# Kernel optimization log

Hardware: AMD Instinct MI355X
Metric: run time of the kernel (lower is better)

The kernel has to match this reference:

```python
import jax, jax.numpy as jnp
import numpy as np

DIM = 512; H = 8; TEMP_LEN = 16; TARGET_LEN = 22
NT = TEMP_LEN ** 2          # 256 temp tokens
NS = TARGET_LEN ** 2        # 484 target tokens
N = NT + NS                 # 740
HD = DIM // H
SCALE = HD ** -0.5
EPS = 1e-5
B = 16


def _bias_index(L):
    coords = np.stack(np.meshgrid(np.arange(L), np.arange(L), indexing='ij')).reshape(2, -1)
    rel = (coords[:, :, None] - coords[:, None, :]).transpose(1, 2, 0)  # [L^2, L^2, 2]
    rel[..., 0] += L - 1
    rel[..., 1] += L - 1
    rel[..., 0] *= 2 * L - 1
    return jnp.asarray(rel.sum(-1))  # [L^2, L^2] indices into (2L-1)^2 table

TEMP_IDX = _bias_index(TEMP_LEN)
TARGET_IDX = _bias_index(TARGET_LEN)


def setup_inputs() -> dict:
    key = jax.random.key(0)
    ctr = iter(range(100))
    def nrm(shape, s=1.0):
        return jax.random.normal(jax.random.fold_in(key, next(ctr)), shape, jnp.float32) * s
    def uni(shape):
        return jax.random.uniform(jax.random.fold_in(key, next(ctr)), shape, jnp.float32, 0.5, 1.5)
    d = {'x': nrm((B, N, DIM))}
    for nm in ('q', 'k', 'v'):
        d[f'conv_{nm}_w'] = nrm((DIM, 1, 3, 3), 0.2)   # depthwise 3x3, groups=DIM
        d[f'bn_{nm}_g'] = 1.0 + nrm((DIM,), 0.1)
        d[f'bn_{nm}_b'] = nrm((DIM,), 0.1)
        d[f'bn_{nm}_m'] = nrm((DIM,), 0.1)
        d[f'bn_{nm}_v'] = uni((DIM,))
    for nm in ('q', 'k', 'v', 'p'):
        d[f'w{nm}'] = nrm((DIM, DIM), DIM ** -0.5)
        d[f'b{nm}'] = nrm((DIM,), 0.01)
    d['rpb_target'] = nrm(((2 * TARGET_LEN - 1) ** 2, H), 0.0002)
    d['rpb_temp'] = nrm(((2 * TEMP_LEN - 1) ** 2, 1), 0.0002)
    d['tt_bias'] = nrm((H, 1, NT), 0.0002)       # temp_target_bias_table
    d['tg_tm_bias'] = nrm((H, NS, 1), 0.0002)    # target_temp_bias_table
    return d


def _dwconv_bn(z, w, g, b, m, v):
    # z: [B, C, Hh, Ww]; depthwise conv + BatchNorm2d (inference stats)
    y = jax.lax.conv_general_dilated(z, w, (1, 1), ((1, 1), (1, 1)),
                                     dimension_numbers=('NCHW', 'OIHW', 'NCHW'),
                                     feature_group_count=DIM)
    inv = (g * jax.lax.rsqrt(v + EPS))[None, :, None, None]
    return (y - m[None, :, None, None]) * inv + b[None, :, None, None]


def reference(x, conv_q_w, bn_q_g, bn_q_b, bn_q_m, bn_q_v,
              conv_k_w, bn_k_g, bn_k_b, bn_k_m, bn_k_v,
              conv_v_w, bn_v_g, bn_v_b, bn_v_m, bn_v_v,
              wq, bq, wk, bk, wv, bv, wp, bp,
              rpb_target, rpb_temp, tt_bias, tg_tm_bias):
    Bb = x.shape[0]
    to_img = lambda t, L: t.transpose(0, 2, 1).reshape(Bb, DIM, L, L)
    to_seq = lambda t: t.reshape(Bb, DIM, -1).transpose(0, 2, 1)
    ti = to_img(x[:, :NT], TEMP_LEN)
    tg = to_img(x[:, NT:], TARGET_LEN)

    def conv_branch(w, g, b, m, v):
        return jnp.concatenate([to_seq(_dwconv_bn(ti, w, g, b, m, v)),
                                to_seq(_dwconv_bn(tg, w, g, b, m, v))], axis=1)

    q = conv_branch(conv_q_w, bn_q_g, bn_q_b, bn_q_m, bn_q_v) @ wq + bq
    k = conv_branch(conv_k_w, bn_k_g, bn_k_b, bn_k_m, bn_k_v) @ wk + bk
    v = conv_branch(conv_v_w, bn_v_g, bn_v_b, bn_v_m, bn_v_v) @ wv + bv

    heads = lambda t: t.reshape(Bb, -1, H, HD).transpose(0, 2, 1, 3)
    qtm, ktm, vtm = heads(q[:, :NT]), heads(k[:, :NT]), heads(v[:, :NT])
    qta, kh, vh = heads(q[:, NT:]), heads(k), heads(v)

    # gathered relative-position bias tables
    target_bias = rpb_target[TARGET_IDX.reshape(-1)].reshape(NS, NS, H).transpose(2, 0, 1)  # [H,NS,NS]
    temp_bias = rpb_temp[TEMP_IDX.reshape(-1)].reshape(NT, NT, 1).transpose(2, 0, 1)        # [1,NT,NT]
    padding = tt_bias + tg_tm_bias                                                          # [H,NS,NT]
    rel = jnp.concatenate([padding, target_bias], axis=2)                                   # [H,NS,N]

    # target -> all attention
    attn = jax.nn.softmax(jnp.einsum('bhqd,bhkd->bhqk', qta, kh) * SCALE + rel, axis=-1)
    out_t = jnp.einsum('bhqk,bhkd->bhqd', attn, vh).transpose(0, 2, 1, 3).reshape(Bb, NS, DIM)

    # temp -> temp attention (bias broadcast over heads)
    attn2 = jax.nn.softmax(jnp.einsum('bhqd,bhkd->bhqk', qtm, ktm) * SCALE + temp_bias, axis=-1)
    out_m = jnp.einsum('bhqk,bhkd->bhqd', attn2, vtm).transpose(0, 2, 1, 3).reshape(Bb, NT, DIM)

    return jnp.concatenate([out_m, out_t], axis=1) @ wp + bp
```

## Files before the change

kernel.cpp:

```cpp
#include <hip/hip_runtime.h>
#include <hip/hip_bf16.h>

typedef unsigned short u16;
typedef unsigned int u32;
typedef __attribute__((ext_vector_type(8))) short short8;
typedef __attribute__((ext_vector_type(4))) float f32x4;

#define NTOK 740
#define NTMP 256
#define NTGT 484
#define DM   512
#define MH   8
#define MROWS 11840
#define KPAD 768
#define LOG2E 1.4426950408889634f

__device__ __forceinline__ float b2f(u16 u) {
    union { unsigned int i; float f; } x; x.i = ((unsigned int)u) << 16; return x.f;
}
__device__ __forceinline__ u16 f2b(float f) {
    union { float f; unsigned int i; } x; x.f = f;
    unsigned int r = x.i + 0x7FFFu + ((x.i >> 16) & 1u);
    return (u16)(r >> 16);
}
__device__ __forceinline__ u32 pk2(float a, float b) {
    union { __hip_bfloat162 h; u32 u; } p;
    p.h = __float22bfloat162_rn(float2{a, b});
    return p.u;
}
__device__ __forceinline__ float fexp2(float x) {
    return __builtin_amdgcn_exp2f(x);
}
struct alignas(8) us4 { u16 x, y, z, w; };

__device__ __forceinline__ void gload16(const void* g, void* l) {
    __builtin_amdgcn_global_load_lds(
        (const __attribute__((address_space(1))) void*)g,
        (__attribute__((address_space(3))) void*)l, 16, 0, 0);
}

__global__ __launch_bounds__(256) void transpose4(const float* __restrict__ w0,
                                                  const float* __restrict__ w1,
                                                  const float* __restrict__ w2,
                                                  const float* __restrict__ w3,
                                                  u16* __restrict__ wTbase) {
    __shared__ float t[32][33];
    const int z = blockIdx.z;
    const float* W = z == 0 ? w0 : z == 1 ? w1 : z == 2 ? w2 : w3;
    u16* WT = wTbase + (size_t)z * 262144;
    int bx = blockIdx.x, by = blockIdx.y;
    int tx = threadIdx.x;
    for (int i = threadIdx.y; i < 32; i += 8)
        t[i][tx] = W[(size_t)(by * 32 + i) * 512 + bx * 32 + tx];
    __syncthreads();
    for (int i = threadIdx.y; i < 32; i += 8)
        WT[(size_t)(bx * 32 + i) * 512 + by * 32 + tx] = f2b(t[tx][i]);
}

__global__ __launch_bounds__(512) void prep_conv3(
    const float* __restrict__ cw0, const float* __restrict__ g0, const float* __restrict__ bb0,
    const float* __restrict__ m0, const float* __restrict__ v0,
    const float* __restrict__ cw1, const float* __restrict__ g1, const float* __restrict__ bb1,
    const float* __restrict__ m1, const float* __restrict__ v1,
    const float* __restrict__ cw2, const float* __restrict__ g2, const float* __restrict__ bb2,
    const float* __restrict__ m2, const float* __restrict__ v2,
    float* __restrict__ cwfb, float* __restrict__ shb) {
    const int tap = blockIdx.x, br = blockIdx.y, c = threadIdx.x;
    const float* cw = br == 0 ? cw0 : br == 1 ? cw1 : cw2;
    const float* g  = br == 0 ? g0  : br == 1 ? g1  : g2;
    const float* bb = br == 0 ? bb0 : br == 1 ? bb1 : bb2;
    const float* m  = br == 0 ? m0  : br == 1 ? m1  : m2;
    const float* v  = br == 0 ? v0  : br == 1 ? v1  : v2;
    const float inv = g[c] * rsqrtf(v[c] + 1e-5f);
    cwfb[(br * 9 + tap) * DM + c] = cw[c * 9 + tap] * inv;
    if (tap == 0) shb[br * DM + c] = bb[c] - m[c] * inv;
}

__global__ __launch_bounds__(256) void conv_bn3(
    const float* __restrict__ x,
    const float* __restrict__ cwfb, const float* __restrict__ shb,
    u16* __restrict__ o0, u16* __restrict__ o1, u16* __restrict__ o2) {
    const int bn = blockIdx.x * 2 + (threadIdx.x >> 7);
    const int c = (threadIdx.x & 127) * 4;
    const int b = bn / NTOK, n = bn % NTOK;
    const bool tmp = n < NTMP;
    const int L = tmp ? 16 : 22, base = tmp ? 0 : NTMP, p = n - base;
    const int ph = p / L, pw = p % L;
    float4 xv[9];
#pragma unroll
    for (int tap = 0; tap < 9; ++tap) {
        const int dh = tap / 3 - 1, dw = tap % 3 - 1;
        const int h2 = ph + dh, w2 = pw + dw;
        const bool ok = (h2 >= 0 && h2 < L && w2 >= 0 && w2 < L);
        xv[tap] = ok ? *(const float4*)(x + (size_t)(b * NTOK + base + h2 * L + w2) * DM + c)
                     : float4{0.f, 0.f, 0.f, 0.f};
    }
    const size_t o = (size_t)bn * DM + c;
    u16* out[3] = {o0, o1, o2};
#pragma unroll
    for (int br = 0; br < 3; ++br) {
        float4 acc = *(const float4*)(shb + br * DM + c);
#pragma unroll
        for (int tap = 0; tap < 9; ++tap) {
            const float4 wv = *(const float4*)(cwfb + (br * 9 + tap) * DM + c);
            acc.x = fmaf(wv.x, xv[tap].x, acc.x);
            acc.y = fmaf(wv.y, xv[tap].y, acc.y);
            acc.z = fmaf(wv.z, xv[tap].z, acc.z);
            acc.w = fmaf(wv.w, xv[tap].w, acc.w);
        }
        us4 r;
        r.x = f2b(acc.x); r.y = f2b(acc.y); r.z = f2b(acc.z); r.w = f2b(acc.w);
        *(us4*)(out[br] + o) = r;
    }
}

#define GEMM_BODY(A, BT)                                                             \
    const int tid = threadIdx.x;                                                     \
    const int gm0 = blockIdx.x * 64;                                                 \
    const int gn0 = blockIdx.y * 128;                                                \
    const int lane = tid & 63, w = tid >> 6;                                         \
    const int lr = lane & 15, lg = lane >> 4;                                        \
    const int wm = (w >> 1) * 32, wn = (w & 1) * 64;                                 \
    const int srow4 = lane >> 2;                                                     \
    const int sc = (lane & 3) ^ (srow4 & 3);                                         \
    const u16* asrc  = A  + (size_t)(gm0 + w * 16 + srow4) * 512 + sc * 8;           \
    const u16* bsrc0 = BT + (size_t)(gn0 + w * 32 + srow4) * 512 + sc * 8;           \
    const u16* bsrc1 = BT + (size_t)(gn0 + w * 32 + 16 + srow4) * 512 + sc * 8;      \
    f32x4 acc[2][4] = {};                                                            \
    gload16(asrc, &As[0][w * 512]);                                                  \
    gload16(bsrc0, &Bs[0][w * 1024]);                                                \
    gload16(bsrc1, &Bs[0][w * 1024 + 512]);                                          \
    for (int kt = 0; kt < 16; ++kt) {                                                \
        const int cur = kt & 1;                                                      \
        if (kt < 15) {                                                               \
            gload16(asrc + (kt + 1) * 32, &As[cur ^ 1][w * 512]);                    \
            gload16(bsrc0 + (kt + 1) * 32, &Bs[cur ^ 1][w * 1024]);                  \
            gload16(bsrc1 + (kt + 1) * 32, &Bs[cur ^ 1][w * 1024 + 512]);            \
            asm volatile("s_waitcnt vmcnt(3)" ::: "memory");                         \
        } else {                                                                     \
            asm volatile("s_waitcnt vmcnt(0)" ::: "memory");                         \
        }                                                                            \
        __syncthreads();                                                             \
        short8 af[2], bfr[4];                                                        \
        _Pragma("unroll")                                                            \
        for (int i = 0; i < 2; ++i)                                                  \
            af[i] = *(const short8*)&As[cur][(wm + i * 16 + lr) * 32 + (lg ^ (lr & 3)) * 8]; \
        _Pragma("unroll")                                                            \
        for (int j = 0; j < 4; ++j)                                                  \
            bfr[j] = *(const short8*)&Bs[cur][(wn + j * 16 + lr) * 32 + (lg ^ (lr & 3)) * 8]; \
        _Pragma("unroll")                                                            \
        for (int i = 0; i < 2; ++i)                                                  \
            _Pragma("unroll")                                                        \
            for (int j = 0; j < 4; ++j)                                              \
                acc[i][j] = __builtin_amdgcn_mfma_f32_16x16x32_bf16(af[i], bfr[j], acc[i][j], 0, 0, 0); \
        __syncthreads();                                                             \
    }

__global__ __launch_bounds__(256) void gemm_qkv(
    const u16* __restrict__ Aq, const u16* __restrict__ Ak, const u16* __restrict__ Av,
    const u16* __restrict__ wTb, const float* __restrict__ bq,
    const float* __restrict__ bk, const float* __restrict__ bv,
    u16* __restrict__ qout, u16* __restrict__ kout, u16* __restrict__ vbT, int zbase) {
    __shared__ u16 As[2][64 * 32];
    __shared__ u16 Bs[2][128 * 32];
    const int z = blockIdx.z + zbase;
    const u16* A = z == 0 ? Aq : z == 1 ? Ak : Av;
    const u16* BT = wTb + (size_t)z * 262144;
    const float* bias = z == 0 ? bq : z == 1 ? bk : bv;
    GEMM_BODY(A, BT)
    u16* lin = z == 0 ? qout : kout;
#pragma unroll
    for (int i = 0; i < 2; ++i)
#pragma unroll
        for (int j = 0; j < 4; ++j) {
            const int gc = gn0 + wn + j * 16 + lr;
            const float bvl = bias[gc];
#pragma unroll
            for (int r = 0; r < 4; ++r) {
                const int gr = gm0 + wm + i * 16 + lg * 4 + r;
                const float val = acc[i][j][r] + bvl;
                if (z == 2) {
                    const int b2 = gr / NTOK, k = gr - b2 * NTOK;
                    const int hh = gc >> 6, d = gc & 63;
                    vbT[((size_t)(b2 * MH + hh) * 64 + d) * KPAD + k] = f2b(val);
                } else {
                    lin[(size_t)gr * 512 + gc] = f2b(val);
                }
            }
        }
}

__global__ __launch_bounds__(256) void gemm_out(const u16* __restrict__ Ain,
                                                const u16* __restrict__ BTin,
                                                const float* __restrict__ bias,
                                                float* __restrict__ C) {
    __shared__ u16 As[2][64 * 32];
    __shared__ u16 Bs[2][128 * 32];
    GEMM_BODY(Ain, BTin)
#pragma unroll
    for (int i = 0; i < 2; ++i)
#pragma unroll
        for (int j = 0; j < 4; ++j) {
            const int gc = gn0 + wn + j * 16 + lr;
            const float bvl = bias[gc];
#pragma unroll
            for (int r = 0; r < 4; ++r) {
                const int gr = gm0 + wm + i * 16 + lg * 4 + r;
                C[(size_t)gr * 512 + gc] = acc[i][j][r] + bvl;
            }
        }
}

__global__ __launch_bounds__(256) void build_bias_t(const float* __restrict__ rpb_t,
                                                    const float* __restrict__ tt,
                                                    const float* __restrict__ tg,
                                                    u16* __restrict__ btab) {
    const int q = blockIdx.x, h = blockIdx.y;
    const int qh = q / 22, qw = q % 22;
    const float tgv = tg[h * NTGT + q];
    for (int k = threadIdx.x; k < KPAD; k += 256) {
        float val;
        if (k < NTMP) val = (tt[h * NTMP + k] + tgv) * LOG2E;
        else if (k < NTOK) {
            const int kj = k - NTMP, kh = kj / 22, kw = kj % 22;
            val = rpb_t[((qh - kh + 21) * 43 + (qw - kw + 21)) * MH + h] * LOG2E;
        } else val = -1e30f;
        btab[((size_t)(h * NTGT + q)) * KPAD + k] = f2b(val);
    }
}
__global__ __launch_bounds__(256) void build_bias_m(const float* __restrict__ rpb_m,
                                                    u16* __restrict__ mtab) {
    const int q = blockIdx.x, k = threadIdx.x;
    const int qh = q >> 4, qw = q & 15, kh = k >> 4, kw = k & 15;
    mtab[q * 256 + k] = f2b(rpb_m[(qh - kh + 15) * 31 + (qw - kw + 15)] * LOG2E);
}

__global__ __launch_bounds__(256) void attn_all(const u16* __restrict__ qb,
                                                const u16* __restrict__ kb,
                                                const u16* __restrict__ vbT,
                                                const u16* __restrict__ btab,
                                                const u16* __restrict__ mtab,
                                                u16* __restrict__ attb) {
    __shared__ u16 Ks[2][32][64];
    __shared__ u16 VTs[2][64][32];
    __shared__ u16 Pb[4][16][32];

    int wg = blockIdx.x + 12 * (blockIdx.y + 8 * blockIdx.z);
    wg = (wg & 7) * 192 + (wg >> 3);
    const int bx = wg % 12;
    const int hb = wg / 12;
    const int h = hb & 7, b = hb >> 3;

    const bool tgt = bx < 8;
    const int q0 = (tgt ? bx : bx - 8) * 64;
    const int NKr = tgt ? NTOK : NTMP;
    const int NCH = tgt ? 24 : 8;
    const int QTOT = tgt ? NTGT : NTMP;
    const int QOFF = tgt ? NTMP : 0;
    const int tid = threadIdx.x;
    const int w = tid >> 6, lane = tid & 63;
    const int lq = lane & 15, lg = lane >> 4;
    const int fq = (lq & 3) ^ ((lq >> 2) & 3);
    const size_t brow = (size_t)b * NTOK;
    const float SCL = 0.125f * LOG2E;

    int qmine = q0 + w * 16 + lq;
    if (qmine > QTOT - 1) qmine = QTOT - 1;
    const u16* trow = tgt ? (btab + ((size_t)(h * NTGT + qmine)) * KPAD)
                          : (mtab + qmine * 256);

    short8 qf[2];
#pragma unroll
    for (int dc = 0; dc < 2; ++dc)
        qf[dc] = *(const short8*)(qb + (brow + QOFF + qmine) * DM + h * 64 + dc * 32 + lg * 8);

    const int krow = tid >> 3, ksc = tid & 7;
    const int vrow = tid >> 2, vsc = tid & 3;
    const int fv = (vrow & 3) ^ ((vrow >> 2) & 3);
    const size_t vbase = (size_t)(b * MH + h) * 64 * KPAD;
    const u16* kptr2 = kb + brow * DM + h * 64 + (ksc ^ (krow & 7)) * 8;
    const u16* vptr2 = vbT + vbase + (size_t)vrow * KPAD + (vsc ^ fv) * 8;
    const int NKm1 = NKr - 1;

    float mrun = -1e30f, lrun = 0.f;
    f32x4 oT[4] = {};

    {
        const int keyc = krow < NKm1 ? krow : NKm1;
        gload16(kptr2 + (size_t)keyc * DM, &Ks[0][w * 8][0]);
        gload16(vptr2, &VTs[0][w * 16][0]);
    }
    us4 bc0 = *(const us4*)(trow + lg * 4);
    us4 bc1 = *(const us4*)(trow + 16 + lg * 4);
    asm volatile("s_waitcnt vmcnt(0)" ::: "memory");
    __syncthreads();

    for (int kc = 0; kc < NCH; ++kc) {
        const int cur = kc & 1, nxt = cur ^ 1;
        const bool more = (kc + 1 < NCH);
        us4 bn0 = {0, 0, 0, 0}, bn1 = {0, 0, 0, 0};
        if (more) {
            const int key = (kc + 1) * 32 + krow;
            const int keyc = key < NKm1 ? key : NKm1;
            gload16(kptr2 + (size_t)keyc * DM, &Ks[nxt][w * 8][0]);
            gload16(vptr2 + (kc + 1) * 32, &VTs[nxt][w * 16][0]);
            bn0 = *(const us4*)(trow + (kc + 1) * 32 + lg * 4);
            bn1 = *(const us4*)(trow + (kc + 1) * 32 + 16 + lg * 4);
        }

        f32x4 s0 = {}, s1 = {};
        __builtin_amdgcn_s_setprio(1);
#pragma unroll
        for (int dc = 0; dc < 2; ++dc) {
            short8 a0 = *(const short8*)&Ks[cur][lq][((dc * 4 + lg) ^ (lq & 7)) * 8];
            short8 a1 = *(const short8*)&Ks[cur][16 + lq][((dc * 4 + lg) ^ (lq & 7)) * 8];
            s0 = __builtin_amdgcn_mfma_f32_16x16x32_bf16(a0, qf[dc], s0, 0, 0, 0);
            s1 = __builtin_amdgcn_mfma_f32_16x16x32_bf16(a1, qf[dc], s1, 0, 0, 0);
        }
        __builtin_amdgcn_s_setprio(0);
        float sv[8];
        sv[0] = fmaf(s0[0], SCL, b2f(bc0.x)); sv[1] = fmaf(s0[1], SCL, b2f(bc0.y));
        sv[2] = fmaf(s0[2], SCL, b2f(bc0.z)); sv[3] = fmaf(s0[3], SCL, b2f(bc0.w));
        sv[4] = fmaf(s1[0], SCL, b2f(bc1.x)); sv[5] = fmaf(s1[1], SCL, b2f(bc1.y));
        sv[6] = fmaf(s1[2], SCL, b2f(bc1.z)); sv[7] = fmaf(s1[3], SCL, b2f(bc1.w));

        float cm = sv[0];
#pragma unroll
        for (int i = 1; i < 8; ++i) cm = fmaxf(cm, sv[i]);
        cm = fmaxf(cm, __shfl_xor(cm, 16));
        cm = fmaxf(cm, __shfl_xor(cm, 32));
        if (!__all(cm <= mrun)) {
            const float mnew = fmaxf(mrun, cm);
            const float alpha = fexp2(mrun - mnew);
#pragma unroll
            for (int t = 0; t < 4; ++t)
#pragma unroll
                for (int r = 0; r < 4; ++r) oT[t][r] *= alpha;
            lrun *= alpha;
            mrun = mnew;
        }
        float pv[8]; float psum = 0.f;
#pragma unroll
        for (int i = 0; i < 8; ++i) { pv[i] = fexp2(sv[i] - mrun); psum += pv[i]; }

        const int c0 = (((lg >> 1) ^ fq) & 3) * 8 + (lg & 1) * 4;
        const int c1 = (((2 + (lg >> 1)) ^ fq) & 3) * 8 + (lg & 1) * 4;
        *(uint2*)&Pb[w][lq][c0] = uint2{pk2(pv[0], pv[1]), pk2(pv[2], pv[3])};
        *(uint2*)&Pb[w][lq][c1] = uint2{pk2(pv[4], pv[5]), pk2(pv[6], pv[7])};

        psum += __shfl_xor(psum, 16);
        psum += __shfl_xor(psum, 32);
        lrun += psum;

        asm volatile("s_waitcnt lgkmcnt(0)" ::: "memory");

        short8 pf = *(const short8*)&Pb[w][lq][((lg ^ fq) & 3) * 8];
        __builtin_amdgcn_s_setprio(1);
#pragma unroll
        for (int t = 0; t < 4; ++t) {
            short8 vf = *(const short8*)&VTs[cur][t * 16 + lq][((lg ^ fq) & 3) * 8];
            oT[t] = __builtin_amdgcn_mfma_f32_16x16x32_bf16(vf, pf, oT[t], 0, 0, 0);
        }
        __builtin_amdgcn_s_setprio(0);

        bc0 = bn0; bc1 = bn1;
        asm volatile("s_waitcnt vmcnt(0)" ::: "memory");
        __syncthreads();
    }

    const float linv = 1.f / lrun;
    const int qrow = q0 + w * 16 + lq;
    if (qrow < QTOT) {
        u16* op = attb + (brow + QOFF + qrow) * DM + h * 64;
#pragma unroll
        for (int t = 0; t < 4; ++t)
            *(uint2*)(op + t * 16 + lg * 4) =
                uint2{pk2(oT[t][0] * linv, oT[t][1] * linv),
                      pk2(oT[t][2] * linv, oT[t][3] * linv)};
    }
}

extern "C" void kernel_launch(void* const* d_in, const int* in_sizes, int n_in,
                              void* d_out, int out_size, void* d_ws, size_t ws_size,
                              hipStream_t stream) {
    const float* x = (const float*)d_in[0];
    const float* convw[3] = {(const float*)d_in[1], (const float*)d_in[6], (const float*)d_in[11]};
    const float* bng[3]   = {(const float*)d_in[2], (const float*)d_in[7], (const float*)d_in[12]};
    const float* bnb[3]   = {(const float*)d_in[3], (const float*)d_in[8], (const float*)d_in[13]};
    const float* bnm[3]   = {(const float*)d_in[4], (const float*)d_in[9], (const float*)d_in[14]};
    const float* bnv[3]   = {(const float*)d_in[5], (const float*)d_in[10], (const float*)d_in[15]};
    const float* w[4]     = {(const float*)d_in[16], (const float*)d_in[18], (const float*)d_in[20], (const float*)d_in[22]};
    const float* bias[4]  = {(const float*)d_in[17], (const float*)d_in[19], (const float*)d_in[21], (const float*)d_in[23]};
    const float* rpb_t = (const float*)d_in[24];
    const float* rpb_m = (const float*)d_in[25];
    const float* tt    = (const float*)d_in[26];
    const float* tg    = (const float*)d_in[27];

    char* ws = (char*)d_ws;
    u16* wTb = (u16*)ws;
    const size_t SEQ = (size_t)MROWS * DM * 2;
    u16* cbq  = (u16*)(ws + 2097152);
    u16* cbk  = (u16*)(ws + 2097152 + SEQ);
    u16* cbv  = (u16*)(ws + 2097152 + 2 * SEQ);
    u16* kbuf = (u16*)(ws + 2097152 + 3 * SEQ);
    u16* vbT  = (u16*)(ws + 2097152 + 4 * SEQ);
    u16* btab = (u16*)(ws + 2097152 + 4 * SEQ + 12582912);
    u16* mtab = (u16*)(ws + 2097152 + 4 * SEQ + 12582912 + 5947392);
    float* cwf = (float*)(ws + 2097152 + 4 * SEQ + 12582912 + 5947392 + 131072);
    float* shf = cwf + 3 * 9 * DM;
    u16* qbuf = cbv;
    u16* attb = cbq;

    transpose4<<<dim3(16, 16, 4), dim3(32, 8), 0, stream>>>(w[0], w[1], w[2], w[3], wTb);
    prep_conv3<<<dim3(9, 3), 512, 0, stream>>>(
        convw[0], bng[0], bnb[0], bnm[0], bnv[0],
        convw[1], bng[1], bnb[1], bnm[1], bnv[1],
        convw[2], bng[2], bnb[2], bnm[2], bnv[2], cwf, shf);
    build_bias_t<<<dim3(NTGT, MH), 256, 0, stream>>>(rpb_t, tt, tg, btab);
    build_bias_m<<<256, 256, 0, stream>>>(rpb_m, mtab);

    conv_bn3<<<MROWS / 2, 256, 0, stream>>>(x, cwf, shf, cbq, cbk, cbv);

    gemm_qkv<<<dim3(185, 4, 1), 256, 0, stream>>>(cbq, cbk, cbv, wTb,
                                                  bias[0], bias[1], bias[2],
                                                  qbuf, kbuf, vbT, 2);
    gemm_qkv<<<dim3(185, 4, 2), 256, 0, stream>>>(cbq, cbk, cbv, wTb,
                                                  bias[0], bias[1], bias[2],
                                                  qbuf, kbuf, vbT, 0);

    attn_all<<<dim3(12, 8, 16), 256, 0, stream>>>(qbuf, kbuf, vbT, btab, mtab, attb);

    gemm_out<<<dim3(185, 4), 256, 0, stream>>>(attb, wTb + 3 * 262144, bias[3], (float*)d_out);
}
```

Measured before the change: 184.6 us.

## Process two 64-query tiles per attention block and merge QKV GEMM launches

Each attention workgroup now handles 128 query rows, two independent 64-row tiles with separate online-softmax state, while sharing the same K/V shared-memory tiles. This halves K/V global loads and LDS staging per query and halves the grid. Separately, when the workspace is large enough, Q goes into its own buffer so the Q, K and V GEMMs can run in one launch instead of two. In exchange the attention kernel uses more registers and has fewer blocks, which may lower occupancy and leave padded rows idle in the last tiles.

```diff
diff --git a/kernel.cpp b/kernel.cpp
--- a/kernel.cpp
+++ b/kernel.cpp
@@ -243,20 +243,21 @@
                                                 u16* __restrict__ attb) {
     __shared__ u16 Ks[2][32][64];
     __shared__ u16 VTs[2][64][32];
-    __shared__ u16 Pb[4][16][32];
-
-    int wg = blockIdx.x + 12 * (blockIdx.y + 8 * blockIdx.z);
-    wg = (wg & 7) * 192 + (wg >> 3);
-    const int bx = wg % 12;
-    const int hb = wg / 12;
+    __shared__ u16 Pb[2][4][16][32];
+
+    int wg = blockIdx.x + 6 * (blockIdx.y + 8 * blockIdx.z);
+    wg = (wg & 7) * 96 + (wg >> 3);
+    const int bx = wg % 6;
+    const int hb = wg / 6;
     const int h = hb & 7, b = hb >> 3;
 
-    const bool tgt = bx < 8;
-    const int q0 = (tgt ? bx : bx - 8) * 64;
+    const bool tgt = bx < 4;
+    const int q0 = (tgt ? bx : bx - 4) * 128;
     const int NKr = tgt ? NTOK : NTMP;
     const int NCH = tgt ? 24 : 8;
     const int QTOT = tgt ? NTGT : NTMP;
     const int QOFF = tgt ? NTMP : 0;
+    const int TK = tgt ? KPAD : 256;
     const int tid = threadIdx.x;
     const int w = tid >> 6, lane = tid & 63;
     const int lq = lane & 15, lg = lane >> 4;
@@ -264,15 +265,18 @@
     const size_t brow = (size_t)b * NTOK;
     const float SCL = 0.125f * LOG2E;
 
-    int qmine = q0 + w * 16 + lq;
-    if (qmine > QTOT - 1) qmine = QTOT - 1;
-    const u16* trow = tgt ? (btab + ((size_t)(h * NTGT + qmine)) * KPAD)
-                          : (mtab + qmine * 256);
-
-    short8 qf[2];
-#pragma unroll
-    for (int dc = 0; dc < 2; ++dc)
-        qf[dc] = *(const short8*)(qb + (brow + QOFF + qmine) * DM + h * 64 + dc * 32 + lg * 8);
+    int qA = q0 + w * 16 + lq;       if (qA > QTOT - 1) qA = QTOT - 1;
+    int qB = q0 + 64 + w * 16 + lq;  if (qB > QTOT - 1) qB = QTOT - 1;
+    const u16* tbase = tgt ? (btab + (size_t)h * NTGT * KPAD) : mtab;
+    const u16* trowA = tbase + (size_t)qA * TK;
+    const u16* trowB = tbase + (size_t)qB * TK;
+
+    short8 qfA[2], qfB[2];
+#pragma unroll
+    for (int dc = 0; dc < 2; ++dc) {
+        qfA[dc] = *(const short8*)(qb + (brow + QOFF + qA) * DM + h * 64 + dc * 32 + lg * 8);
+        qfB[dc] = *(const short8*)(qb + (brow + QOFF + qB) * DM + h * 64 + dc * 32 + lg * 8);
+    }
 
     const int krow = tid >> 3, ksc = tid & 7;
     const int vrow = tid >> 2, vsc = tid & 3;
@@ -282,101 +286,155 @@
     const u16* vptr2 = vbT + vbase + (size_t)vrow * KPAD + (vsc ^ fv) * 8;
     const int NKm1 = NKr - 1;
 
-    float mrun = -1e30f, lrun = 0.f;
-    f32x4 oT[4] = {};
+    float mrunA = -1e30f, lrunA = 0.f, mrunB = -1e30f, lrunB = 0.f;
+    f32x4 oTA[4] = {}, oTB[4] = {};
 
     {
         const int keyc = krow < NKm1 ? krow : NKm1;
         gload16(kptr2 + (size_t)keyc * DM, &Ks[0][w * 8][0]);
         gload16(vptr2, &VTs[0][w * 16][0]);
     }
-    us4 bc0 = *(const us4*)(trow + lg * 4);
-    us4 bc1 = *(const us4*)(trow + 16 + lg * 4);
+    us4 bcA0 = *(const us4*)(trowA + lg * 4);
+    us4 bcA1 = *(const us4*)(trowA + 16 + lg * 4);
+    us4 bcB0 = *(const us4*)(trowB + lg * 4);
+    us4 bcB1 = *(const us4*)(trowB + 16 + lg * 4);
     asm volatile("s_waitcnt vmcnt(0)" ::: "memory");
     __syncthreads();
 
     for (int kc = 0; kc < NCH; ++kc) {
         const int cur = kc & 1, nxt = cur ^ 1;
         const bool more = (kc + 1 < NCH);
-        us4 bn0 = {0, 0, 0, 0}, bn1 = {0, 0, 0, 0};
+        us4 bnA0 = {0,0,0,0}, bnA1 = {0,0,0,0}, bnB0 = {0,0,0,0}, bnB1 = {0,0,0,0};
         if (more) {
             const int key = (kc + 1) * 32 + krow;
             const int keyc = key < NKm1 ? key : NKm1;
             gload16(kptr2 + (size_t)keyc * DM, &Ks[nxt][w * 8][0]);
             gload16(vptr2 + (kc + 1) * 32, &VTs[nxt][w * 16][0]);
-            bn0 = *(const us4*)(trow + (kc + 1) * 32 + lg * 4);
-            bn1 = *(const us4*)(trow + (kc + 1) * 32 + 16 + lg * 4);
-        }
-
-        f32x4 s0 = {}, s1 = {};
+            bnA0 = *(const us4*)(trowA + (kc + 1) * 32 + lg * 4);
+            bnA1 = *(const us4*)(trowA + (kc + 1) * 32 + 16 + lg * 4);
+            bnB0 = *(const us4*)(trowB + (kc + 1) * 32 + lg * 4);
+            bnB1 = *(const us4*)(trowB + (kc + 1) * 32 + 16 + lg * 4);
+        }
+
+        f32x4 sA0 = {}, sA1 = {}, sB0 = {}, sB1 = {};
         __builtin_amdgcn_s_setprio(1);
 #pragma unroll
         for (int dc = 0; dc < 2; ++dc) {
             short8 a0 = *(const short8*)&Ks[cur][lq][((dc * 4 + lg) ^ (lq & 7)) * 8];
             short8 a1 = *(const short8*)&Ks[cur][16 + lq][((dc * 4 + lg) ^ (lq & 7)) * 8];
-            s0 = __builtin_amdgcn_mfma_f32_16x16x32_bf16(a0, qf[dc], s0, 0, 0, 0);
-            s1 = __builtin_amdgcn_mfma_f32_16x16x32_bf16(a1, qf[dc], s1, 0, 0, 0);
+            sA0 = __builtin_amdgcn_mfma_f32_16x16x32_bf16(a0, qfA[dc], sA0, 0, 0, 0);
+            sB0 = __builtin_amdgcn_mfma_f32_16x16x32_bf16(a0, qfB[dc], sB0, 0, 0, 0);
+            sA1 = __builtin_amdgcn_mfma_f32_16x16x32_bf16(a1, qfA[dc], sA1, 0, 0, 0);
+            sB1 = __builtin_amdgcn_mfma_f32_16x16x32_bf16(a1, qfB[dc], sB1, 0, 0, 0);
         }
         __builtin_amdgcn_s_setprio(0);
-        float sv[8];
-        sv[0] = fmaf(s0[0], SCL, b2f(bc0.x)); sv[1] = fmaf(s0[1], SCL, b2f(bc0.y));
-        sv[2] = fmaf(s0[2], SCL, b2f(bc0.z)); sv[3] = fmaf(s0[3], SCL, b2f(bc0.w));
-        sv[4] = fmaf(s1[0], SCL, b2f(bc1.x)); sv[5] = fmaf(s1[1], SCL, b2f(bc1.y));
-        sv[6] = fmaf(s1[2], SCL, b2f(bc1.z)); sv[7] = fmaf(s1[3], SCL, b2f(bc1.w));
-
-        float cm = sv[0];
-#pragma unroll
-        for (int i = 1; i < 8; ++i) cm = fmaxf(cm, sv[i]);
-        cm = fmaxf(cm, __shfl_xor(cm, 16));
-        cm = fmaxf(cm, __shfl_xor(cm, 32));
-        if (!__all(cm <= mrun)) {
-            const float mnew = fmaxf(mrun, cm);
-            const float alpha = fexp2(mrun - mnew);
-#pragma unroll
-            for (int t = 0; t < 4; ++t)
-#pragma unroll
-                for (int r = 0; r < 4; ++r) oT[t][r] *= alpha;
-            lrun *= alpha;
-            mrun = mnew;
-        }
-        float pv[8]; float psum = 0.f;
-#pragma unroll
-        for (int i = 0; i < 8; ++i) { pv[i] = fexp2(sv[i] - mrun); psum += pv[i]; }
-
-        const int c0 = (((lg >> 1) ^ fq) & 3) * 8 + (lg & 1) * 4;
-        const int c1 = (((2 + (lg >> 1)) ^ fq) & 3) * 8 + (lg & 1) * 4;
-        *(uint2*)&Pb[w][lq][c0] = uint2{pk2(pv[0], pv[1]), pk2(pv[2], pv[3])};
-        *(uint2*)&Pb[w][lq][c1] = uint2{pk2(pv[4], pv[5]), pk2(pv[6], pv[7])};
-
-        psum += __shfl_xor(psum, 16);
-        psum += __shfl_xor(psum, 32);
-        lrun += psum;
+
+        {
+            float sv[8];
+            sv[0] = fmaf(sA0[0], SCL, b2f(bcA0.x)); sv[1] = fmaf(sA0[1], SCL, b2f(bcA0.y));
+            sv[2] = fmaf(sA0[2], SCL, b2f(bcA0.z)); sv[3] = fmaf(sA0[3], SCL, b2f(bcA0.w));
+            sv[4] = fmaf(sA1[0], SCL, b2f(bcA1.x)); sv[5] = fmaf(sA1[1], SCL, b2f(bcA1.y));
+            sv[6] = fmaf(sA1[2], SCL, b2f(bcA1.z)); sv[7] = fmaf(sA1[3], SCL, b2f(bcA1.w));
+            float cm = sv[0];
+#pragma unroll
+            for (int i = 1; i < 8; ++i) cm = fmaxf(cm, sv[i]);
+            cm = fmaxf(cm, __shfl_xor(cm, 16));
+            cm = fmaxf(cm, __shfl_xor(cm, 32));
+            if (!__all(cm <= mrunA)) {
+                const float mnew = fmaxf(mrunA, cm);
+                const float alpha = fexp2(mrunA - mnew);
+#pragma unroll
+                for (int t = 0; t < 4; ++t)
+#pragma unroll
+                    for (int r = 0; r < 4; ++r) oTA[t][r] *= alpha;
+                lrunA *= alpha;
+                mrunA = mnew;
+            }
+            float pv[8], psum = 0.f;
+#pragma unroll
+            for (int i = 0; i < 8; ++i) { pv[i] = fexp2(sv[i] - mrunA); psum += pv[i]; }
+            const int c0 = (((lg >> 1) ^ fq) & 3) * 8 + (lg & 1) * 4;
+            const int c1 = (((2 + (lg >> 1)) ^ fq) & 3) * 8 + (lg & 1) * 4;
+            *(uint2*)&Pb[0][w][lq][c0] = uint2{pk2(pv[0], pv[1]), pk2(pv[2], pv[3])};
+            *(uint2*)&Pb[0][w][lq][c1] = uint2{pk2(pv[4], pv[5]), pk2(pv[6], pv[7])};
+            psum += __shfl_xor(psum, 16);
+            psum += __shfl_xor(psum, 32);
+            lrunA += psum;
+        }
+        {
+            float sv[8];
+            sv[0] = fmaf(sB0[0], SCL, b2f(bcB0.x)); sv[1] = fmaf(sB0[1], SCL, b2f(bcB0.y));
+            sv[2] = fmaf(sB0[2], SCL, b2f(bcB0.z)); sv[3] = fmaf(sB0[3], SCL, b2f(bcB0.w));
+            sv[4] = fmaf(sB1[0], SCL, b2f(bcB1.x)); sv[5] = fmaf(sB1[1], SCL, b2f(bcB1.y));
+            sv[6] = fmaf(sB1[2], SCL, b2f(bcB1.z)); sv[7] = fmaf(sB1[3], SCL, b2f(bcB1.w));
+            float cm = sv[0];
+#pragma unroll
+            for (int i = 1; i < 8; ++i) cm = fmaxf(cm, sv[i]);
+            cm = fmaxf(cm, __shfl_xor(cm, 16));
+            cm = fmaxf(cm, __shfl_xor(cm, 32));
+            if (!__all(cm <= mrunB)) {
+                const float mnew = fmaxf(mrunB, cm);
+                const float alpha = fexp2(mrunB - mnew);
+#pragma unroll
+                for (int t = 0; t < 4; ++t)
+#pragma unroll
+                    for (int r = 0; r < 4; ++r) oTB[t][r] *= alpha;
+                lrunB *= alpha;
+                mrunB = mnew;
+            }
+            float pv[8], psum = 0.f;
+#pragma unroll
+            for (int i = 0; i < 8; ++i) { pv[i] = fexp2(sv[i] - mrunB); psum += pv[i]; }
+            const int c0 = (((lg >> 1) ^ fq) & 3) * 8 + (lg & 1) * 4;
+            const int c1 = (((2 + (lg >> 1)) ^ fq) & 3) * 8 + (lg & 1) * 4;
+            *(uint2*)&Pb[1][w][lq][c0] = uint2{pk2(pv[0], pv[1]), pk2(pv[2], pv[3])};
+            *(uint2*)&Pb[1][w][lq][c1] = uint2{pk2(pv[4], pv[5]), pk2(pv[6], pv[7])};
+            psum += __shfl_xor(psum, 16);
+            psum += __shfl_xor(psum, 32);
+            lrunB += psum;
+        }
 
         asm volatile("s_waitcnt lgkmcnt(0)" ::: "memory");
 
-        short8 pf = *(const short8*)&Pb[w][lq][((lg ^ fq) & 3) * 8];
+        short8 pfA = *(const short8*)&Pb[0][w][lq][((lg ^ fq) & 3) * 8];
+        short8 pfB = *(const short8*)&Pb[1][w][lq][((lg ^ fq) & 3) * 8];
         __builtin_amdgcn_s_setprio(1);
 #pragma unroll
         for (int t = 0; t < 4; ++t) {
             short8 vf = *(const short8*)&VTs[cur][t * 16 + lq][((lg ^ fq) & 3) * 8];
-            oT[t] = __builtin_amdgcn_mfma_f32_16x16x32_bf16(vf, pf, oT[t], 0, 0, 0);
+            oTA[t] = __builtin_amdgcn_mfma_f32_16x16x32_bf16(vf, pfA, oTA[t], 0, 0, 0);
+            oTB[t] = __builtin_amdgcn_mfma_f32_16x16x32_bf16(vf, pfB, oTB[t], 0, 0, 0);
         }
         __builtin_amdgcn_s_setprio(0);
 
-        bc0 = bn0; bc1 = bn1;
+        bcA0 = bnA0; bcA1 = bnA1; bcB0 = bnB0; bcB1 = bnB1;
         asm volatile("s_waitcnt vmcnt(0)" ::: "memory");
         __syncthreads();
     }
 
-    const float linv = 1.f / lrun;
-    const int qrow = q0 + w * 16 + lq;
-    if (qrow < QTOT) {
-        u16* op = attb + (brow + QOFF + qrow) * DM + h * 64;
-#pragma unroll
-        for (int t = 0; t < 4; ++t)
-            *(uint2*)(op + t * 16 + lg * 4) =
-                uint2{pk2(oT[t][0] * linv, oT[t][1] * linv),
-                      pk2(oT[t][2] * linv, oT[t][3] * linv)};
+    {
+        const float linv = 1.f / lrunA;
+        const int qrow = q0 + w * 16 + lq;
+        if (qrow < QTOT) {
+            u16* op = attb + (brow + QOFF + qrow) * DM + h * 64;
+#pragma unroll
+            for (int t = 0; t < 4; ++t)
+                *(uint2*)(op + t * 16 + lg * 4) =
+                    uint2{pk2(oTA[t][0] * linv, oTA[t][1] * linv),
+                          pk2(oTA[t][2] * linv, oTA[t][3] * linv)};
+        }
+    }
+    {
+        const float linv = 1.f / lrunB;
+        const int qrow = q0 + 64 + w * 16 + lq;
+        if (qrow < QTOT) {
+            u16* op = attb + (brow + QOFF + qrow) * DM + h * 64;
+#pragma unroll
+            for (int t = 0; t < 4; ++t)
+                *(uint2*)(op + t * 16 + lg * 4) =
+                    uint2{pk2(oTB[t][0] * linv, oTB[t][1] * linv),
+                          pk2(oTB[t][2] * linv, oTB[t][3] * linv)};
+        }
     }
 }
 
@@ -408,7 +466,9 @@
     u16* mtab = (u16*)(ws + 2097152 + 4 * SEQ + 12582912 + 5947392);
     float* cwf = (float*)(ws + 2097152 + 4 * SEQ + 12582912 + 5947392 + 131072);
     float* shf = cwf + 3 * 9 * DM;
-    u16* qbuf = cbv;
+    const size_t off_q2 = 2097152 + 4 * SEQ + 12582912 + 5947392 + 131072 + 61440;
+    const bool merged = ws_size >= off_q2 + SEQ;
+    u16* qbuf = merged ? (u16*)(ws + off_q2) : cbv;
     u16* attb = cbq;
 
     transpose4<<<dim3(16, 16, 4), dim3(32, 8), 0, stream>>>(w[0], w[1], w[2], w[3], wTb);
@@ -421,14 +481,20 @@
 
     conv_bn3<<<MROWS / 2, 256, 0, stream>>>(x, cwf, shf, cbq, cbk, cbv);
 
-    gemm_qkv<<<dim3(185, 4, 1), 256, 0, stream>>>(cbq, cbk, cbv, wTb,
-                                                  bias[0], bias[1], bias[2],
-                                                  qbuf, kbuf, vbT, 2);
-    gemm_qkv<<<dim3(185, 4, 2), 256, 0, stream>>>(cbq, cbk, cbv, wTb,
-                                                  bias[0], bias[1], bias[2],
-                                                  qbuf, kbuf, vbT, 0);
-
-    attn_all<<<dim3(12, 8, 16), 256, 0, stream>>>(qbuf, kbuf, vbT, btab, mtab, attb);
+    if (merged) {
+        gemm_qkv<<<dim3(185, 4, 3), 256, 0, stream>>>(cbq, cbk, cbv, wTb,
+                                                      bias[0], bias[1], bias[2],
+                                                      qbuf, kbuf, vbT, 0);
+    } else {
+        gemm_qkv<<<dim3(185, 4, 1), 256, 0, stream>>>(cbq, cbk, cbv, wTb,
+                                                      bias[0], bias[1], bias[2],
+                                                      qbuf, kbuf, vbT, 2);
+        gemm_qkv<<<dim3(185, 4, 2), 256, 0, stream>>>(cbq, cbk, cbv, wTb,
+                                                      bias[0], bias[1], bias[2],
+                                                      qbuf, kbuf, vbT, 0);
+    }
+
+    attn_all<<<dim3(6, 8, 16), 256, 0, stream>>>(qbuf, kbuf, vbT, btab, mtab, attb);
 
     gemm_out<<<dim3(185, 4), 256, 0, stream>>>(attb, wTb + 3 * 262144, bias[3], (float*)d_out);
 }
```

New measurement: 179.1 us. 3.0% less time.
